# Kernel optimization log

Measured on AMD Instinct MI355X. Metric: run time of the kernel, lower is better.

Reference implementation:

```python
import jax, jax.numpy as jnp
import numpy as np

BATCH = 2048
OBS_DIM = 48
H0, H1, H2 = 512, 256, 128
ACT_DIM = 12
NUM_TEACHERS = 64


def setup_inputs() -> dict:
    key = jax.random.key(0)
    ks = jax.random.split(key, 10)
    s = lambda fan_in: 1.0 / np.sqrt(fan_in)
    return {
        "obs": jax.random.normal(ks[0], (BATCH, OBS_DIM), dtype=jnp.float32),
        "teacher_indices": jax.random.randint(ks[1], (BATCH,), 0, NUM_TEACHERS),
        "w0": jax.random.normal(ks[2], (NUM_TEACHERS, H0, OBS_DIM), dtype=jnp.float32) * s(OBS_DIM),
        "b0": jax.random.normal(ks[3], (NUM_TEACHERS, H0), dtype=jnp.float32) * s(OBS_DIM),
        "w2": jax.random.normal(ks[4], (NUM_TEACHERS, H1, H0), dtype=jnp.float32) * s(H0),
        "b2": jax.random.normal(ks[5], (NUM_TEACHERS, H1), dtype=jnp.float32) * s(H0),
        "w4": jax.random.normal(ks[6], (NUM_TEACHERS, H2, H1), dtype=jnp.float32) * s(H1),
        "b4": jax.random.normal(ks[7], (NUM_TEACHERS, H2), dtype=jnp.float32) * s(H1),
        "w6": jax.random.normal(ks[8], (NUM_TEACHERS, ACT_DIM, H2), dtype=jnp.float32) * s(H2),
        "b6": jax.random.normal(ks[9], (NUM_TEACHERS, ACT_DIM), dtype=jnp.float32) * s(H2),
    }


def reference(obs, teacher_indices, w0, b0, w2, b2, w4, b4, w6, b6):
    # Per-sample gather of full teacher layer weights, then batched GEMV.
    def layer(x, w, b):
        # x: [B, in]; w[idx]: [B, out, in]; b[idx]: [B, out]
        return jnp.einsum("boi,bi->bo", w[teacher_indices], x) + b[teacher_indices]

    x = jax.nn.elu(layer(obs, w0, b0))
    x = jax.nn.elu(layer(x, w2, b2))
    x = jax.nn.elu(layer(x, w4, b4))
    x = jnp.tanh(layer(x, w6, b6))
    return x
```

## Files before the change

kernel.cpp:

```cpp
#include <hip/hip_runtime.h>

#define BATCH 2048
#define NTEACH 64

typedef __attribute__((ext_vector_type(8))) short short8;
typedef __attribute__((ext_vector_type(4))) float f32x4;

__device__ __forceinline__ unsigned short f2bf(float f) {
    unsigned u = __float_as_uint(f);
    u += 0x7FFFu + ((u >> 16) & 1u);
    return (unsigned short)(u >> 16);
}

__device__ __forceinline__ short8 cvt8(float4 a, float4 b) {
    short8 r;
    r[0] = (short)f2bf(a.x); r[1] = (short)f2bf(a.y);
    r[2] = (short)f2bf(a.z); r[3] = (short)f2bf(a.w);
    r[4] = (short)f2bf(b.x); r[5] = (short)f2bf(b.y);
    r[6] = (short)f2bf(b.z); r[7] = (short)f2bf(b.w);
    return r;
}

__global__ __launch_bounds__(256) void sort_kernel(const int* __restrict__ tidx,
                                                   int* __restrict__ offsets,
                                                   int* __restrict__ order) {
    __shared__ int cnt[NTEACH];
    __shared__ int offs[NTEACH + 1];
    __shared__ int cur[NTEACH];
    int tid = threadIdx.x;
    if (tid < NTEACH) cnt[tid] = 0;
    __syncthreads();
    for (int i = tid; i < BATCH; i += 256) atomicAdd(&cnt[tidx[i]], 1);
    __syncthreads();
    if (tid == 0) {
        int a = 0;
        for (int t = 0; t < NTEACH; ++t) { offs[t] = a; a += cnt[t]; }
        offs[NTEACH] = a;
    }
    __syncthreads();
    if (tid < NTEACH) cur[tid] = offs[tid];
    if (tid < NTEACH + 1) offsets[tid] = offs[tid];
    __syncthreads();
    for (int i = tid; i < BATCH; i += 256) {
        int p = atomicAdd(&cur[tidx[i]], 1);
        order[p] = i;
    }
}

__global__ __launch_bounds__(256) void gather_kernel(const float* __restrict__ obs,
                                                     const int* __restrict__ order,
                                                     unsigned short* __restrict__ obs_s) {
    int gtid = blockIdx.x * 256 + threadIdx.x;
    int r = gtid >> 3;
    int c0 = (gtid & 7) * 8;
    short8 v = {0, 0, 0, 0, 0, 0, 0, 0};
    if (c0 < 48) {
        const float* src = obs + (size_t)order[r] * 48 + c0;
        float4 a = *reinterpret_cast<const float4*>(src);
        float4 b = *reinterpret_cast<const float4*>(src + 4);
        v = cvt8(a, b);
    }
    *reinterpret_cast<short8*>(&obs_s[(size_t)r * 64 + c0]) = v;
}

template <int K, int KVALID, int NOUT>
__global__ __launch_bounds__(256) void layer_mfma(const unsigned short* __restrict__ xs,
                                                  const float* __restrict__ W,
                                                  const float* __restrict__ Bv,
                                                  const int* __restrict__ offsets,
                                                  unsigned short* __restrict__ ys) {
    constexpr int KT = K / 32;
    const int t = blockIdx.y;
    const int start = offsets[t];
    const int end = offsets[t + 1];
    if (start >= end) return;
    const int w = threadIdx.x >> 6;
    const int l = threadIdx.x & 63;
    const int ln = l & 15;
    const int kg = l >> 4;
    const int n0 = blockIdx.x * 64 + w * 16;

    short8 bfrag[KT];
    const float* wrow = W + ((size_t)t * NOUT + n0 + ln) * KVALID;
#pragma unroll
    for (int kt = 0; kt < KT; ++kt) {
        int kb = kt * 32 + kg * 8;
        short8 f = {0, 0, 0, 0, 0, 0, 0, 0};
        if (kb < KVALID) {
            float4 a = *reinterpret_cast<const float4*>(wrow + kb);
            float4 b = *reinterpret_cast<const float4*>(wrow + kb + 4);
            f = cvt8(a, b);
        }
        bfrag[kt] = f;
    }
    const float bias = Bv[(size_t)t * NOUT + n0 + ln];

    for (int r0 = start; r0 < end; r0 += 16) {
        f32x4 acc = {0.f, 0.f, 0.f, 0.f};
        const unsigned short* xrow = xs + (size_t)(r0 + ln) * K + kg * 8;
#pragma unroll
        for (int kt = 0; kt < KT; ++kt) {
            short8 af = *reinterpret_cast<const short8*>(xrow + kt * 32);
            acc = __builtin_amdgcn_mfma_f32_16x16x32_bf16(af, bfrag[kt], acc, 0, 0, 0);
        }
#pragma unroll
        for (int j = 0; j < 4; ++j) {
            int m = kg * 4 + j;
            if (r0 + m < end) {
                float v = acc[j] + bias;
                v = v > 0.f ? v : expm1f(v);
                ys[(size_t)(r0 + m) * NOUT + n0 + ln] = f2bf(v);
            }
        }
    }
}

__global__ __launch_bounds__(256) void final_mfma(const unsigned short* __restrict__ xs,
                                                  const float* __restrict__ W,
                                                  const float* __restrict__ Bv,
                                                  const int* __restrict__ offsets,
                                                  const int* __restrict__ order,
                                                  float* __restrict__ out) {
    constexpr int K = 128, KT = 4, NOUT = 12;
    const int t = blockIdx.x;
    const int start = offsets[t];
    const int end = offsets[t + 1];
    const int w = threadIdx.x >> 6;
    const int l = threadIdx.x & 63;
    const int ln = l & 15;
    const int kg = l >> 4;
    const bool nvalid = ln < NOUT;

    short8 bfrag[KT];
    const float* wrow = W + ((size_t)t * NOUT + (nvalid ? ln : 0)) * K;
#pragma unroll
    for (int kt = 0; kt < KT; ++kt) {
        int kb = kt * 32 + kg * 8;
        float4 a = *reinterpret_cast<const float4*>(wrow + kb);
        float4 b = *reinterpret_cast<const float4*>(wrow + kb + 4);
        bfrag[kt] = cvt8(a, b);
    }
    const float bias = nvalid ? Bv[(size_t)t * NOUT + ln] : 0.f;

    for (int mt = w;; mt += 4) {
        int r0 = start + mt * 16;
        if (r0 >= end) break;
        f32x4 acc = {0.f, 0.f, 0.f, 0.f};
        const unsigned short* xrow = xs + (size_t)(r0 + ln) * K + kg * 8;
#pragma unroll
        for (int kt = 0; kt < KT; ++kt) {
            short8 af = *reinterpret_cast<const short8*>(xrow + kt * 32);
            acc = __builtin_amdgcn_mfma_f32_16x16x32_bf16(af, bfrag[kt], acc, 0, 0, 0);
        }
        if (nvalid) {
#pragma unroll
            for (int j = 0; j < 4; ++j) {
                int m = kg * 4 + j;
                if (r0 + m < end)
                    out[(size_t)order[r0 + m] * NOUT + ln] = tanhf(acc[j] + bias);
            }
        }
    }
}

extern "C" void kernel_launch(void* const* d_in, const int* in_sizes, int n_in,
                              void* d_out, int out_size, void* d_ws, size_t ws_size,
                              hipStream_t stream) {
    const float* obs = (const float*)d_in[0];
    const int* tidx  = (const int*)d_in[1];
    const float* w0  = (const float*)d_in[2];
    const float* b0  = (const float*)d_in[3];
    const float* w2  = (const float*)d_in[4];
    const float* b2  = (const float*)d_in[5];
    const float* w4  = (const float*)d_in[6];
    const float* b4  = (const float*)d_in[7];
    const float* w6  = (const float*)d_in[8];
    const float* b6  = (const float*)d_in[9];
    float* out = (float*)d_out;

    const int ROWS = BATCH + 16;
    char* ws = (char*)d_ws;
    int* offsets = (int*)ws;
    int* order   = (int*)(ws + 1024);
    unsigned short* obs_s = (unsigned short*)(ws + 16384);
    unsigned short* h0 = obs_s + (size_t)ROWS * 64;
    unsigned short* h1 = h0 + (size_t)ROWS * 512;
    unsigned short* h2 = h1 + (size_t)ROWS * 256;

    sort_kernel<<<1, 256, 0, stream>>>(tidx, offsets, order);
    gather_kernel<<<64, 256, 0, stream>>>(obs, order, obs_s);
    layer_mfma<64, 48, 512><<<dim3(8, NTEACH), 256, 0, stream>>>(obs_s, w0, b0, offsets, h0);
    layer_mfma<512, 512, 256><<<dim3(4, NTEACH), 256, 0, stream>>>(h0, w2, b2, offsets, h1);
    layer_mfma<256, 256, 128><<<dim3(2, NTEACH), 256, 0, stream>>>(h1, w4, b4, offsets, h2);
    final_mfma<<<NTEACH, 256, 0, stream>>>(h2, w6, b6, offsets, order, out);
}
```

Measured before the change: 48.08 us.

## Fuse obs gather into first layer and split K/M across waves

Removes the separate gather kernel: the first layer now reads fp32 obs rows through the sort order and converts them to bf16 in-register. The layer kernel is generalized so the four waves of a block can split K (with an LDS reduction), N, or M. Layers 2 and 3 use a 4-way K split with four times as many blocks, raising occupancy and shortening each wave's serial weight load. The sort kernel uses 1024 threads. In exchange, the K-split layers add two block barriers and an LDS reduction per 16-row tile, and the workspace row padding grows.

Result: faster. 39.36 us (-18.1%).

```diff
diff --git a/kernel.cpp b/kernel.cpp
--- a/kernel.cpp
+++ b/kernel.cpp
@@ -21,16 +21,16 @@
     return r;
 }
 
-__global__ __launch_bounds__(256) void sort_kernel(const int* __restrict__ tidx,
-                                                   int* __restrict__ offsets,
-                                                   int* __restrict__ order) {
+__global__ __launch_bounds__(1024) void sort_kernel(const int* __restrict__ tidx,
+                                                    int* __restrict__ offsets,
+                                                    int* __restrict__ order) {
     __shared__ int cnt[NTEACH];
     __shared__ int offs[NTEACH + 1];
     __shared__ int cur[NTEACH];
     int tid = threadIdx.x;
     if (tid < NTEACH) cnt[tid] = 0;
     __syncthreads();
-    for (int i = tid; i < BATCH; i += 256) atomicAdd(&cnt[tidx[i]], 1);
+    for (int i = tid; i < BATCH; i += 1024) atomicAdd(&cnt[tidx[i]], 1);
     __syncthreads();
     if (tid == 0) {
         int a = 0;
@@ -41,52 +41,49 @@
     if (tid < NTEACH) cur[tid] = offs[tid];
     if (tid < NTEACH + 1) offsets[tid] = offs[tid];
     __syncthreads();
-    for (int i = tid; i < BATCH; i += 256) {
+    for (int i = tid; i < BATCH; i += 1024) {
         int p = atomicAdd(&cur[tidx[i]], 1);
         order[p] = i;
     }
 }
 
-__global__ __launch_bounds__(256) void gather_kernel(const float* __restrict__ obs,
-                                                     const int* __restrict__ order,
-                                                     unsigned short* __restrict__ obs_s) {
-    int gtid = blockIdx.x * 256 + threadIdx.x;
-    int r = gtid >> 3;
-    int c0 = (gtid & 7) * 8;
-    short8 v = {0, 0, 0, 0, 0, 0, 0, 0};
-    if (c0 < 48) {
-        const float* src = obs + (size_t)order[r] * 48 + c0;
-        float4 a = *reinterpret_cast<const float4*>(src);
-        float4 b = *reinterpret_cast<const float4*>(src + 4);
-        v = cvt8(a, b);
-    }
-    *reinterpret_cast<short8*>(&obs_s[(size_t)r * 64 + c0]) = v;
-}
-
-template <int K, int KVALID, int NOUT>
-__global__ __launch_bounds__(256) void layer_mfma(const unsigned short* __restrict__ xs,
+template <int K, int KVALID, int NOUT, int KSPLIT, int NSPLIT, int MSPLIT,
+          bool GATHER, bool IS_ELU>
+__global__ __launch_bounds__(256) void layer_mfma(const void* __restrict__ xin,
                                                   const float* __restrict__ W,
                                                   const float* __restrict__ Bv,
                                                   const int* __restrict__ offsets,
+                                                  const int* __restrict__ order,
                                                   unsigned short* __restrict__ ys) {
-    constexpr int KT = K / 32;
+    constexpr int KSL = K / KSPLIT;
+    constexpr int KTW = KSL / 32;
+    static_assert(KSL % 32 == 0, "K slice");
+    static_assert(KSPLIT * NSPLIT * MSPLIT == 4, "4 waves");
+    static_assert(KSPLIT == 1 || MSPLIT == 1, "barrier uniformity");
+
+    __shared__ f32x4 red[4][64];
+
     const int t = blockIdx.y;
     const int start = offsets[t];
     const int end = offsets[t + 1];
     if (start >= end) return;
-    const int w = threadIdx.x >> 6;
+    const int wid = threadIdx.x >> 6;
     const int l = threadIdx.x & 63;
     const int ln = l & 15;
     const int kg = l >> 4;
-    const int n0 = blockIdx.x * 64 + w * 16;
-
-    short8 bfrag[KT];
-    const float* wrow = W + ((size_t)t * NOUT + n0 + ln) * KVALID;
-#pragma unroll
-    for (int kt = 0; kt < KT; ++kt) {
+    const int kq = wid % KSPLIT;
+    const int nq = (wid / KSPLIT) % NSPLIT;
+    const int mq = wid / (KSPLIT * NSPLIT);
+    const int n0 = blockIdx.x * (16 * NSPLIT) + nq * 16;
+    const int kbase = kq * KSL;
+
+    short8 bfrag[KTW];
+    const float* wrow = W + ((size_t)t * NOUT + n0 + ln) * KVALID + kbase;
+#pragma unroll
+    for (int kt = 0; kt < KTW; ++kt) {
         int kb = kt * 32 + kg * 8;
         short8 f = {0, 0, 0, 0, 0, 0, 0, 0};
-        if (kb < KVALID) {
+        if (kbase + kb < KVALID) {
             float4 a = *reinterpret_cast<const float4*>(wrow + kb);
             float4 b = *reinterpret_cast<const float4*>(wrow + kb + 4);
             f = cvt8(a, b);
@@ -95,21 +92,52 @@
     }
     const float bias = Bv[(size_t)t * NOUT + n0 + ln];
 
-    for (int r0 = start; r0 < end; r0 += 16) {
+    for (int r0 = start + mq * 16; r0 < end; r0 += 16 * MSPLIT) {
         f32x4 acc = {0.f, 0.f, 0.f, 0.f};
-        const unsigned short* xrow = xs + (size_t)(r0 + ln) * K + kg * 8;
-#pragma unroll
-        for (int kt = 0; kt < KT; ++kt) {
-            short8 af = *reinterpret_cast<const short8*>(xrow + kt * 32);
-            acc = __builtin_amdgcn_mfma_f32_16x16x32_bf16(af, bfrag[kt], acc, 0, 0, 0);
-        }
-#pragma unroll
-        for (int j = 0; j < 4; ++j) {
-            int m = kg * 4 + j;
-            if (r0 + m < end) {
-                float v = acc[j] + bias;
-                v = v > 0.f ? v : expm1f(v);
-                ys[(size_t)(r0 + m) * NOUT + n0 + ln] = f2bf(v);
+        if (GATHER) {
+            int rr = (r0 + ln < end) ? order[r0 + ln] : order[start];
+            const float* xr = (const float*)xin + (size_t)rr * KVALID + kbase;
+#pragma unroll
+            for (int kt = 0; kt < KTW; ++kt) {
+                int kb = kt * 32 + kg * 8;
+                short8 af = {0, 0, 0, 0, 0, 0, 0, 0};
+                if (kbase + kb < KVALID) {
+                    float4 a = *reinterpret_cast<const float4*>(xr + kb);
+                    float4 b = *reinterpret_cast<const float4*>(xr + kb + 4);
+                    af = cvt8(a, b);
+                }
+                acc = __builtin_amdgcn_mfma_f32_16x16x32_bf16(af, bfrag[kt], acc, 0, 0, 0);
+            }
+        } else {
+            const unsigned short* xr =
+                (const unsigned short*)xin + (size_t)(r0 + ln) * K + kbase + kg * 8;
+#pragma unroll
+            for (int kt = 0; kt < KTW; ++kt) {
+                short8 af = *reinterpret_cast<const short8*>(xr + kt * 32);
+                acc = __builtin_amdgcn_mfma_f32_16x16x32_bf16(af, bfrag[kt], acc, 0, 0, 0);
+            }
+        }
+        if (KSPLIT > 1) {
+            __syncthreads();
+            if (kq > 0) red[wid][l] = acc;
+            __syncthreads();
+            if (kq == 0) {
+#pragma unroll
+                for (int s = 1; s < KSPLIT; ++s) {
+                    f32x4 r = red[wid + s][l];
+                    acc[0] += r[0]; acc[1] += r[1]; acc[2] += r[2]; acc[3] += r[3];
+                }
+            }
+        }
+        if (kq == 0) {
+#pragma unroll
+            for (int j = 0; j < 4; ++j) {
+                int m = kg * 4 + j;
+                if (r0 + m < end) {
+                    float v = acc[j] + bias;
+                    if (IS_ELU) v = v > 0.f ? v : expm1f(v);
+                    ys[(size_t)(r0 + m) * NOUT + n0 + ln] = f2bf(v);
+                }
             }
         }
     }
@@ -178,19 +206,20 @@
     const float* b6  = (const float*)d_in[9];
     float* out = (float*)d_out;
 
-    const int ROWS = BATCH + 16;
+    const int ROWS = BATCH + 64;
     char* ws = (char*)d_ws;
     int* offsets = (int*)ws;
     int* order   = (int*)(ws + 1024);
-    unsigned short* obs_s = (unsigned short*)(ws + 16384);
-    unsigned short* h0 = obs_s + (size_t)ROWS * 64;
+    unsigned short* h0 = (unsigned short*)(ws + 16384);
     unsigned short* h1 = h0 + (size_t)ROWS * 512;
     unsigned short* h2 = h1 + (size_t)ROWS * 256;
 
-    sort_kernel<<<1, 256, 0, stream>>>(tidx, offsets, order);
-    gather_kernel<<<64, 256, 0, stream>>>(obs, order, obs_s);
-    layer_mfma<64, 48, 512><<<dim3(8, NTEACH), 256, 0, stream>>>(obs_s, w0, b0, offsets, h0);
-    layer_mfma<512, 512, 256><<<dim3(4, NTEACH), 256, 0, stream>>>(h0, w2, b2, offsets, h1);
-    layer_mfma<256, 256, 128><<<dim3(2, NTEACH), 256, 0, stream>>>(h1, w4, b4, offsets, h2);
+    sort_kernel<<<1, 1024, 0, stream>>>(tidx, offsets, order);
+    layer_mfma<64, 48, 512, 1, 2, 2, true, true>
+        <<<dim3(16, NTEACH), 256, 0, stream>>>(obs, w0, b0, offsets, order, h0);
+    layer_mfma<512, 512, 256, 4, 1, 1, false, true>
+        <<<dim3(16, NTEACH), 256, 0, stream>>>(h0, w2, b2, offsets, order, h1);
+    layer_mfma<256, 256, 128, 4, 1, 1, false, true>
+        <<<dim3(8, NTEACH), 256, 0, stream>>>(h1, w4, b4, offsets, order, h2);
     final_mfma<<<NTEACH, 256, 0, stream>>>(h2, w6, b6, offsets, order, out);
 }
```
